# Optimization experiments

Hardware: AMD Instinct MI355X
Metric: run time of the kernel (lower is better)

## Reference

```python
import jax, jax.numpy as jnp
import numpy as np

B = 1
H_IMG, W_IMG = 64, 64
NF = H_IMG * W_IMG          # 4096 front/query tokens
NS = 1024                   # satellite tokens (32x32 grid)
SAT_IN, FRONT_IN = 768, 320
NH, HD = 8, 64
MD = NH * HD                # 512
GHID, GHD = 128, 16
GMD = NH * GHD              # 128
GEO_RATIO, ROPE_BASE = 0.5, 10000.0
LAMBDA_GEO, LAMBDA_GEOM = 1.0, 1.0
EPS = 1e-5


def _linear(x, w, b):
    return x @ w.T + b


def _layernorm(x, g, b):
    m = x.mean(-1, keepdims=True)
    v = jnp.var(x, axis=-1, keepdims=True)
    return (x - m) / jnp.sqrt(v + EPS) * g + b


def _georope(t, xy):
    """Continuous 2D (x,y) rotary embedding on the first GEO_RATIO fraction of head_dim.
    t: [B,NH,N,HD], xy: [B,N,2]."""
    rot = int(HD * GEO_RATIO)       # rotated dims (32)
    axis = rot // 2                 # dims per spatial axis (16)
    half = axis // 2                # frequency pairs per axis (8)
    inv_freq = ROPE_BASE ** (-jnp.arange(half, dtype=t.dtype) / half)

    def rot_axis(a, coord):
        th = coord[:, None, :, None] * inv_freq   # [B,1,N,half]
        c, s = jnp.cos(th), jnp.sin(th)
        a1, a2 = a[..., :half], a[..., half:]
        return jnp.concatenate([a1 * c - a2 * s, a1 * s + a2 * c], axis=-1)

    tx = rot_axis(t[..., :axis], xy[..., 0])
    ty = rot_axis(t[..., axis:rot], xy[..., 1])
    return jnp.concatenate([tx, ty, t[..., rot:]], axis=-1)


def _heads(x, hd):
    b, n, _ = x.shape
    return x.reshape(b, n, NH, hd).transpose(0, 2, 1, 3)


def setup_inputs() -> dict:
    key = jax.random.key(0)
    ks = iter(jax.random.split(key, 64))

    def w(*shape):
        return jax.random.normal(next(ks), shape, jnp.float32) / np.sqrt(shape[-1]).astype(np.float32)

    z = lambda n: jnp.zeros((n,), jnp.float32)
    o = lambda n: jnp.ones((n,), jnp.float32)
    return {
        "front_feat": jax.random.normal(next(ks), (B, FRONT_IN, H_IMG, W_IMG), jnp.float32),
        "front_bev_xy": jax.random.uniform(next(ks), (B, NF, 2), jnp.float32, -1.0, 1.0),
        "sat_tokens": jax.random.normal(next(ks), (B, NS, SAT_IN), jnp.float32),
        "sat_xy": jax.random.uniform(next(ks), (B, NS, 2), jnp.float32, -1.0, 1.0),
        "front_plucker": jax.random.normal(next(ks), (B, NF, 6), jnp.float32),
        "pos_w1": w(MD, 2), "pos_b1": z(MD), "pos_w2": w(MD, MD), "pos_b2": z(MD),
        "fa_w": w(MD, FRONT_IN), "fa_b": z(MD), "fa_ln_g": o(MD), "fa_ln_b": z(MD),
        "qn_g": o(MD), "qn_b": z(MD),
        "sa_w": w(MD, SAT_IN), "sa_b": z(MD), "sa_ln_g": o(MD), "sa_ln_b": z(MD),
        "wq": w(MD, MD), "bq": z(MD), "wk": w(MD, MD), "bk": z(MD), "wv": w(MD, MD), "bv": z(MD),
        "plk_w1": w(GHID, 6), "plk_b1": z(GHID), "plk_w2": w(GHID, GHID), "plk_b2": z(GHID),
        "sxy_w1": w(GHID, 2), "sxy_b1": z(GHID), "sxy_w2": w(GHID, GHID), "sxy_b2": z(GHID),
        "gqn_g": o(GHID), "gqn_b": z(GHID), "gkn_g": o(GHID), "gkn_b": z(GHID),
        "wqg": w(GMD, GHID), "bqg": z(GMD), "wkg": w(GMD, GHID), "bkg": z(GMD),
    }


def reference(front_feat, front_bev_xy, sat_tokens, sat_xy, front_plucker,
              pos_w1, pos_b1, pos_w2, pos_b2, fa_w, fa_b, fa_ln_g, fa_ln_b,
              qn_g, qn_b, sa_w, sa_b, sa_ln_g, sa_ln_b, wq, bq, wk, bk, wv, bv,
              plk_w1, plk_b1, plk_w2, plk_b2, sxy_w1, sxy_b1, sxy_w2, sxy_b2,
              gqn_g, gqn_b, gkn_g, gkn_b, wqg, bqg, wkg, bkg):
    b = front_feat.shape[0]
    ff = front_feat.reshape(b, FRONT_IN, NF).transpose(0, 2, 1)      # [B,NF,C]
    pos = _linear(jax.nn.silu(_linear(front_bev_xy, pos_w1, pos_b1)), pos_w2, pos_b2)
    feat = _layernorm(_linear(ff, fa_w, fa_b), fa_ln_g, fa_ln_b)
    q_embed = _layernorm(pos + feat, qn_g, qn_b)
    sat_feat = _layernorm(_linear(sat_tokens, sa_w, sa_b), sa_ln_g, sa_ln_b)
    q = _heads(_linear(q_embed, wq, bq), HD)                         # [B,H,NF,HD]
    k = _heads(_linear(sat_feat, wk, bk), HD)                        # [B,H,NS,HD]
    v = _heads(_linear(sat_feat, wv, bv), HD)
    qr = _georope(q, front_bev_xy)
    kr = _georope(k, sat_xy)
    logits = jnp.einsum('bhqd,bhkd->bhqk', qr, kr) / np.float32(np.sqrt(HD))
    # learned geometric Q/K stream (Plucker rays vs sat xy)
    plk = _layernorm(_linear(jax.nn.silu(_linear(front_plucker, plk_w1, plk_b1)), plk_w2, plk_b2), gqn_g, gqn_b)
    sgf = _layernorm(_linear(jax.nn.silu(_linear(sat_xy, sxy_w1, sxy_b1)), sxy_w2, sxy_b2), gkn_g, gkn_b)
    qg = _heads(_linear(plk, wqg, bqg), GHD)
    kg = _heads(_linear(sgf, wkg, bkg), GHD)
    logits = logits + LAMBDA_GEOM * (jnp.einsum('bhqd,bhkd->bhqk', qg, kg) / np.float32(np.sqrt(GHD)))
    # additive pairwise squared-distance bias, broadcast over heads
    dist2 = ((front_bev_xy[:, :, None, :] - sat_xy[:, None, :, :]) ** 2).sum(-1)   # [B,NF,NS]
    logits = logits - LAMBDA_GEO * dist2[:, None]
    attn = jax.nn.softmax(logits, axis=-1)
    read = jnp.einsum('bhqk,bhkd->bhqd', attn, v)
    return read.transpose(0, 2, 1, 3).reshape(b, NF, MD)
```

## Files before the change

kernel.cpp:

```cpp
#include <hip/hip_runtime.h>
#include <hip/hip_bf16.h>
#include <stdint.h>

#define NF 4096
#define NS 1024
#define MD 512
#define HD 64
#define DA 96
#define GHID 128

#define L2E 1.44269504f
#define S2L 1.6986436f

typedef unsigned short u16;
typedef __attribute__((ext_vector_type(8))) short bf8v;
typedef __attribute__((ext_vector_type(4))) float f4v;

__device__ __forceinline__ u16 f2bf(float f) {
  __hip_bfloat16 h = __float2bfloat16(f);
  return __builtin_bit_cast(u16, h);
}
__device__ __forceinline__ float bf2f(u16 u) {
  union { unsigned u; float f; } v; v.u = ((unsigned)u) << 16; return v.f;
}
__device__ __forceinline__ f4v mfma16(bf8v a, bf8v b, f4v c) {
  return __builtin_amdgcn_mfma_f32_16x16x32_bf16(a, b, c, 0, 0, 0);
}
__device__ __forceinline__ void gld16(const void* g, void* l) {
  __builtin_amdgcn_global_load_lds(
      (const __attribute__((address_space(1))) unsigned int*)g,
      (__attribute__((address_space(3))) unsigned int*)l, 16, 0, 0);
}

#define OFF_POSW2 0
#define OFF_FAW   262144
#define OFF_SAW   425984
#define OFF_WQ    819200
#define OFF_WKV   1081344
#define OFF_PLKW2 1605632
#define OFF_SXYW2 1622016
#define OFF_WQG   1638400
#define OFF_WKG   1654784
#define OFF_SATT  1671168
#define TOTW      2457600

__global__ __launch_bounds__(256) void k_l0(
    const float* __restrict__ s0, const float* __restrict__ s1,
    const float* __restrict__ s2, const float* __restrict__ s3,
    const float* __restrict__ s4, const float* __restrict__ s5,
    const float* __restrict__ s6, const float* __restrict__ s7,
    const float* __restrict__ s8, const float* __restrict__ s9,
    const float* __restrict__ s10, u16* __restrict__ pool,
    const float* __restrict__ bk, const float* __restrict__ bv,
    float* __restrict__ bkv,
    const float* __restrict__ ff, u16* __restrict__ ffT,
    const float* __restrict__ in0, const float* __restrict__ w0,
    const float* __restrict__ b0, u16* __restrict__ o0,
    const float* __restrict__ in1, const float* __restrict__ w1,
    const float* __restrict__ b1, u16* __restrict__ o1,
    const float* __restrict__ in2, const float* __restrict__ w2,
    const float* __restrict__ b2, u16* __restrict__ o2) {
  __shared__ u16 sT[32][72];
  int blk = blockIdx.x, t = threadIdx.x;
  if (blk < 2401) {
    int i4 = blk * 256 + t;
    if (i4 < TOTW / 4) {
      int idx = i4 * 4;
      const float* src; int off;
      if      (idx < OFF_FAW)   { src = s0;  off = OFF_POSW2; }
      else if (idx < OFF_SAW)   { src = s1;  off = OFF_FAW; }
      else if (idx < OFF_WQ)    { src = s2;  off = OFF_SAW; }
      else if (idx < OFF_WKV)   { src = s3;  off = OFF_WQ; }
      else if (idx < 1343488)   { src = s4;  off = OFF_WKV; }
      else if (idx < OFF_PLKW2) { src = s5;  off = 1343488; }
      else if (idx < OFF_SXYW2) { src = s6;  off = OFF_PLKW2; }
      else if (idx < OFF_WQG)   { src = s7;  off = OFF_SXYW2; }
      else if (idx < OFF_WKG)   { src = s8;  off = OFF_WQG; }
      else if (idx < OFF_SATT)  { src = s9;  off = OFF_WKG; }
      else                      { src = s10; off = OFF_SATT; }
      float4 v = *(const float4*)(src + (idx - off));
      ushort4 o;
      o.x = f2bf(v.x); o.y = f2bf(v.y); o.z = f2bf(v.z); o.w = f2bf(v.w);
      *(ushort4*)(pool + idx) = o;
    } else if (i4 < TOTW / 4 + 256) {
      int j = (i4 - TOTW / 4) * 4;
#pragma unroll
      for (int e = 0; e < 4; ++e) {
        int b = j + e;
        bkv[b] = (b < 512) ? bk[b] : bv[b - 512];
      }
    }
  } else if (blk < 3041) {
    int lb = blk - 2401;
    int n0 = (lb & 63) * 64, c0 = (lb >> 6) * 32;
    {
      int cr = t >> 3, nc = (t & 7) * 8;
      const float* src = ff + (size_t)(c0 + cr) * NF + n0 + nc;
      float4 v0 = *(const float4*)src, v1 = *(const float4*)(src + 4);
      bf8v p;
      p[0]=(short)f2bf(v0.x); p[1]=(short)f2bf(v0.y); p[2]=(short)f2bf(v0.z); p[3]=(short)f2bf(v0.w);
      p[4]=(short)f2bf(v1.x); p[5]=(short)f2bf(v1.y); p[6]=(short)f2bf(v1.z); p[7]=(short)f2bf(v1.w);
      *(bf8v*)&sT[cr][nc] = p;
    }
    __syncthreads();
    {
      int r = t >> 2, cc = (t & 3) * 8;
      bf8v p;
#pragma unroll
      for (int e = 0; e < 8; ++e) p[e] = (short)sT[cc + e][r];
      *(bf8v*)(ffT + (size_t)(n0 + r) * 320 + c0 + cc) = p;
    }
  } else {
    int lb = blk - 3041;
    const float *in, *w, *b; u16* o; int mlog, K, idx;
    if (lb < 8192)       { in = in0; w = w0; b = b0; o = o0; mlog = 9; K = 2; idx = lb * 256 + t; }
    else if (lb < 10240) { in = in1; w = w1; b = b1; o = o1; mlog = 7; K = 6; idx = (lb - 8192) * 256 + t; }
    else                 { in = in2; w = w2; b = b2; o = o2; mlog = 7; K = 2; idx = (lb - 10240) * 256 + t; }
    int M = 1 << mlog;
    int n = idx >> mlog, m = idx & (M - 1);
    float acc = b[m];
    for (int k = 0; k < K; ++k) acc += in[n * K + k] * w[m * K + k];
    o[idx] = f2bf(acc / (1.f + __expf(-acc)));
  }
}

__device__ __forceinline__ void gemm_body(const u16* __restrict__ A, const u16* __restrict__ W,
                                          const float* __restrict__ bias, u16* __restrict__ out,
                                          int m0, int n0, int N, int K) {
  constexpr int BM = 64, BN = 64;
  constexpr int MR = 2, NR = 2;
  __shared__ u16 sA[2][BM * 64];
  __shared__ u16 sB[2][BN * 64];
  const int tid = threadIdx.x, w = tid >> 6, lane = tid & 63;
  const int l16 = lane & 15, lh = lane >> 4;
  const int wr = w >> 1, wc = w & 1;

  f4v acc[MR][NR];
#pragma unroll
  for (int m = 0; m < MR; ++m)
#pragma unroll
    for (int j = 0; j < NR; ++j) acc[m][j] = (f4v){0.f, 0.f, 0.f, 0.f};

  auto stageA = [&](int buf, int k0) {
#pragma unroll
    for (int i = 0; i < 2; ++i) {
      int c = i * 256 + tid;
      int row = c >> 3, cp = c & 7;
      int sc_ = cp ^ (row & 7);
      gld16(A + (size_t)(m0 + row) * K + k0 + sc_ * 8, &sA[buf][c * 8]);
    }
  };
  auto stageB = [&](int buf, int k0) {
#pragma unroll
    for (int i = 0; i < 2; ++i) {
      int c = i * 256 + tid;
      int row = c >> 3, cp = c & 7;
      int sc_ = cp ^ (row & 7);
      gld16(W + (size_t)(n0 + row) * K + k0 + sc_ * 8, &sB[buf][c * 8]);
    }
  };

  stageA(0, 0); stageB(0, 0);
  __syncthreads();
  const int NK = K >> 6;
  for (int ks = 0; ks < NK; ++ks) {
    int nb = ks & 1;
    if (ks + 1 < NK) { stageA(nb ^ 1, (ks + 1) * 64); stageB(nb ^ 1, (ks + 1) * 64); }
#pragma unroll
    for (int kk = 0; kk < 2; ++kk) {
      bf8v af[MR], bfr[NR];
#pragma unroll
      for (int m = 0; m < MR; ++m) {
        int row = wr * 32 + m * 16 + l16;
        int cp = (kk * 4 + lh) ^ (row & 7);
        af[m] = *(const bf8v*)&sA[nb][row * 64 + cp * 8];
      }
#pragma unroll
      for (int j = 0; j < NR; ++j) {
        int row = wc * 32 + j * 16 + l16;
        int cp = (kk * 4 + lh) ^ (row & 7);
        bfr[j] = *(const bf8v*)&sB[nb][row * 64 + cp * 8];
      }
#pragma unroll
      for (int m = 0; m < MR; ++m)
#pragma unroll
        for (int j = 0; j < NR; ++j) acc[m][j] = mfma16(af[m], bfr[j], acc[m][j]);
    }
    __syncthreads();
  }
#pragma unroll
  for (int m = 0; m < MR; ++m) {
    int grow = m0 + wr * 32 + m * 16 + (lh << 2);
#pragma unroll
    for (int j = 0; j < NR; ++j) {
      int gcol = n0 + wc * 32 + j * 16 + l16;
      float bv = bias ? bias[gcol] : 0.f;
#pragma unroll
      for (int r = 0; r < 4; ++r)
        out[(size_t)(grow + r) * N + gcol] = f2bf(acc[m][j][r] + bv);
    }
  }
}

struct GP { const u16* A; const u16* W; const float* bias; u16* out; int K; int N; int M; };

__device__ __forceinline__ void gemm_dispatch(const GP& g, int blk) {
  int mt = g.M >> 6;
  int m0 = (blk % mt) * 64, n0 = (blk / mt) * 64;
  gemm_body(g.A, g.W, g.bias, g.out, m0, n0, g.N, g.K);
}

__global__ __launch_bounds__(256) void k_gemm_L1(GP a, GP b, GP c, GP d, GP e) {
  int blk = blockIdx.x;
  if (blk < 512)       gemm_dispatch(a, blk);
  else if (blk < 1024) gemm_dispatch(b, blk - 512);
  else if (blk < 1152) gemm_dispatch(c, blk - 1024);
  else if (blk < 1280) gemm_dispatch(d, blk - 1152);
  else                 gemm_dispatch(e, blk - 1280);
}
__global__ __launch_bounds__(256) void k_gemm_L2(GP a, GP b, GP c, GP d) {
  int blk = blockIdx.x;
  if (blk < 512)      gemm_dispatch(a, blk);
  else if (blk < 768) gemm_dispatch(b, blk - 512);
  else if (blk < 896) gemm_dispatch(c, blk - 768);
  else                gemm_dispatch(d, blk - 896);
}

__global__ __launch_bounds__(256) void k_ln_all(
    const u16* __restrict__ feat_pre, const u16* __restrict__ pos,
    const float* __restrict__ fg, const float* __restrict__ fb,
    const float* __restrict__ qg, const float* __restrict__ qb2,
    u16* __restrict__ q_embed,
    const u16* __restrict__ satf_pre, const float* __restrict__ sg,
    const float* __restrict__ sb, u16* __restrict__ satf,
    const u16* __restrict__ ginq, const u16* __restrict__ gink,
    const float* __restrict__ ggq, const float* __restrict__ gbq,
    const float* __restrict__ ggk, const float* __restrict__ gbk,
    u16* __restrict__ goutq, u16* __restrict__ goutk) {
  int blk = blockIdx.x;
  int w = threadIdx.x >> 6, lane = threadIdx.x & 63;
  if (blk < 1024) {
    int row = blk * 4 + w;
    bf8v v = *(const bf8v*)(feat_pre + (size_t)row * 512 + lane * 8);
    float x[8];
#pragma unroll
    for (int e = 0; e < 8; ++e) x[e] = bf2f((u16)v[e]);
    float s = 0.f, q = 0.f;
#pragma unroll
    for (int e = 0; e < 8; ++e) { s += x[e]; q += x[e] * x[e]; }
#pragma unroll
    for (int mm = 1; mm < 64; mm <<= 1) { s += __shfl_xor(s, mm); q += __shfl_xor(q, mm); }
    float mean = s / 512.f, var = q / 512.f - mean * mean;
    float rstd = rsqrtf(var + 1e-5f);
    bf8v vp = *(const bf8v*)(pos + (size_t)row * 512 + lane * 8);
#pragma unroll
    for (int e = 0; e < 8; ++e)
      x[e] = (x[e] - mean) * rstd * fg[lane * 8 + e] + fb[lane * 8 + e] + bf2f((u16)vp[e]);
    s = 0.f; q = 0.f;
#pragma unroll
    for (int e = 0; e < 8; ++e) { s += x[e]; q += x[e] * x[e]; }
#pragma unroll
    for (int mm = 1; mm < 64; mm <<= 1) { s += __shfl_xor(s, mm); q += __shfl_xor(q, mm); }
    mean = s / 512.f; var = q / 512.f - mean * mean;
    rstd = rsqrtf(var + 1e-5f);
    bf8v ov;
#pragma unroll
    for (int e = 0; e < 8; ++e)
      ov[e] = (short)f2bf((x[e] - mean) * rstd * qg[lane * 8 + e] + qb2[lane * 8 + e]);
    *(bf8v*)(q_embed + (size_t)row * 512 + lane * 8) = ov;
  } else if (blk < 1280) {
    int row = (blk - 1024) * 4 + w;
    bf8v v = *(const bf8v*)(satf_pre + (size_t)row * 512 + lane * 8);
    float x[8];
#pragma unroll
    for (int e = 0; e < 8; ++e) x[e] = bf2f((u16)v[e]);
    float s = 0.f, q = 0.f;
#pragma unroll
    for (int e = 0; e < 8; ++e) { s += x[e]; q += x[e] * x[e]; }
#pragma unroll
    for (int mm = 1; mm < 64; mm <<= 1) { s += __shfl_xor(s, mm); q += __shfl_xor(q, mm); }
    float mean = s / 512.f, var = q / 512.f - mean * mean;
    float rstd = rsqrtf(var + 1e-5f);
    bf8v ov;
#pragma unroll
    for (int e = 0; e < 8; ++e)
      ov[e] = (short)f2bf((x[e] - mean) * rstd * sg[lane * 8 + e] + sb[lane * 8 + e]);
    *(bf8v*)(satf + (size_t)row * 512 + lane * 8) = ov;
  } else {
    int row = (blk - 1280) * 4 + w;
    const u16* in; const float *g, *b; u16* out;
    if (row < 4096) { in = ginq; g = ggq; b = gbq; out = goutq; }
    else { row -= 4096; in = gink; g = ggk; b = gbk; out = goutk; }
    uint32_t v = *(const uint32_t*)(in + (size_t)row * 128 + lane * 2);
    float x0 = bf2f((u16)(v & 0xffff)), x1 = bf2f((u16)(v >> 16));
    float s = x0 + x1, q = x0 * x0 + x1 * x1;
#pragma unroll
    for (int mm = 1; mm < 64; mm <<= 1) { s += __shfl_xor(s, mm); q += __shfl_xor(q, mm); }
    float mean = s / 128.f, var = q / 128.f - mean * mean;
    float rstd = rsqrtf(var + 1e-5f);
    u16 o0 = f2bf((x0 - mean) * rstd * g[lane * 2] + b[lane * 2]);
    u16 o1 = f2bf((x1 - mean) * rstd * g[lane * 2 + 1] + b[lane * 2 + 1]);
    *(uint32_t*)(out + (size_t)row * 128 + lane * 2) = (uint32_t)o0 | ((uint32_t)o1 << 16);
  }
}

__global__ __launch_bounds__(256) void k_prep(
    const u16* __restrict__ qlin, const u16* __restrict__ qglin,
    const float* __restrict__ qxy, u16* __restrict__ Qaug_,
    const u16* __restrict__ klin, const u16* __restrict__ kglin,
    const float* __restrict__ kxy, u16* __restrict__ Kaug_,
    float* __restrict__ kk2_, u16* __restrict__ VT) {
  __shared__ u16 sT[64][72];
  int blk = blockIdx.x;
  if (blk < 10240) {
    int gid = blk * 4 + (threadIdx.x >> 6);
    int lane = threadIdx.x & 63;
    const u16 *lin, *glin; const float* xy; u16* aug;
    int lstride, n, h, isQ; float scm, scg;
    if (gid < NF * 8) {
      lin = qlin; glin = qglin; xy = qxy; aug = Qaug_;
      lstride = MD; n = gid >> 3; h = gid & 7; isQ = 1;
      scm = 0.125f * L2E; scg = 0.25f * L2E;
    } else {
      gid -= NF * 8;
      lin = klin; glin = kglin; xy = kxy; aug = Kaug_;
      lstride = 1024; n = gid >> 3; h = gid & 7; isQ = 0;
      scm = 1.f; scg = 1.f;
    }
    float val = bf2f(lin[(size_t)n * lstride + h * 64 + lane]);
    float part = __shfl_xor(val, 8);
    float x = xy[n * 2], y = xy[n * 2 + 1];
    float outv = val;
    if (lane < 32) {
      float coord = (lane < 16) ? x : y;
      int j = lane & 7;
      float th = coord * __expf(-(float)j * 1.1512925465f);
      float sn, cs;
      __sincosf(th, &sn, &cs);
      outv = ((lane & 8) == 0) ? (val * cs - part * sn) : (part * sn + val * cs);
    }
    u16* dst = aug + (size_t)(h * (isQ ? NF : NS) + n) * DA;
    dst[lane] = f2bf(outv * scm);
    if (lane < 16) {
      float gv = bf2f(glin[(size_t)n * GHID + h * 16 + lane]);
      dst[64 + lane] = f2bf(gv * scg);
    } else if (lane == 16) {
      dst[80] = f2bf(S2L * x);
    } else if (lane == 17) {
      dst[81] = f2bf(S2L * y);
    } else if (lane == 18) {
      dst[82] = 0;
      if (!isQ && h == 0) kk2_[n] = L2E * (x * x + y * y);
    } else if (lane < 32) {
      dst[64 + lane] = 0;
    }
  } else {
    int lb = blk - 10240;
    int n0 = (lb & 15) * 64, h = lb >> 4;
    int t = threadIdx.x;
    int r = t >> 2, c = (t & 3) * 16;
    const u16* src = klin + (size_t)(n0 + r) * 1024 + 512 + h * 64 + c;
    *(bf8v*)&sT[r][c]     = *(const bf8v*)src;
    *(bf8v*)&sT[r][c + 8] = *(const bf8v*)(src + 8);
    __syncthreads();
    int d = t >> 2, nc = (t & 3) * 16;
    bf8v p0, p1;
#pragma unroll
    for (int e = 0; e < 8; ++e) { p0[e] = (short)sT[nc + e][d]; p1[e] = (short)sT[nc + 8 + e][d]; }
    u16* dst = VT + (size_t)(h * 64 + d) * 1024 + n0 + nc;
    *(bf8v*)dst = p0;
    *(bf8v*)(dst + 8) = p1;
  }
}

__global__ __launch_bounds__(256, 4) void k_flash(const u16* __restrict__ Qa,
                                                  const u16* __restrict__ Ka,
                                                  const u16* __restrict__ VT,
                                                  const float* __restrict__ kk2,
                                                  float* __restrict__ Opart,
                                                  float2* __restrict__ ml) {
  const int h = blockIdx.y, qb = blockIdx.x, sp = blockIdx.z;
  const int tid = threadIdx.x, w = tid >> 6, lane = tid & 63;
  const int l16 = lane & 15, lh = lane >> 4;
  __shared__ u16 sK[64][104];
  __shared__ u16 sV[64][72];
  __shared__ u16 sP[4][16][72];
  __shared__ float sKK[512];

  ((float2*)sKK)[tid] = ((const float2*)(kk2 + sp * 512))[tid];

  const int qrow = qb * 64 + w * 16 + l16;
  bf8v qf[3];
#pragma unroll
  for (int c = 0; c < 3; ++c)
    qf[c] = *(const bf8v*)(Qa + (size_t)(h * NF + qrow) * DA + c * 32 + lh * 8);

  bf8v ONES;
#pragma unroll
  for (int i = 0; i < 8; ++i) ONES[i] = (short)0x3F80;

  const int crow = qb * 64 + w * 16 + (lh << 2);
  float m_run[4], l_run[4];
  f4v accO[4];
#pragma unroll
  for (int r = 0; r < 4; ++r) { m_run[r] = -1e30f; l_run[r] = 0.f; }
#pragma unroll
  for (int d = 0; d < 4; ++d) accO[d] = (f4v){0.f, 0.f, 0.f, 0.f};

  const int kt0 = sp * 8;
  bf8v kreg[3], vreg[2];
  auto sload = [&](int t8) {
    int kb = (kt0 + t8) * 64;
#pragma unroll
    for (int i = 0; i < 3; ++i) {
      int c = tid + i * 256; int r = c / 12, off = (c % 12) * 8;
      kreg[i] = *(const bf8v*)(Ka + ((size_t)(h * NS) + kb + r) * DA + off);
    }
#pragma unroll
    for (int i = 0; i < 2; ++i) {
      int c = tid + i * 256; int d = c >> 3, off = (c & 7) * 8;
      vreg[i] = *(const bf8v*)(VT + ((size_t)(h * HD) + d) * NS + kb + off);
    }
  };
  auto swrite = [&]() {
#pragma unroll
    for (int i = 0; i < 3; ++i) {
      int c = tid + i * 256; int r = c / 12, off = (c % 12) * 8;
      *(bf8v*)&sK[r][off] = kreg[i];
    }
#pragma unroll
    for (int i = 0; i < 2; ++i) {
      int c = tid + i * 256; int d = c >> 3, off = (c & 7) * 8;
      *(bf8v*)&sV[d][off] = vreg[i];
    }
  };

  sload(0); swrite();
  __syncthreads();
  for (int t8 = 0; t8 < 8; ++t8) {
    if (t8 < 7) sload(t8 + 1);
    float p[4][4];
    float rmax[4] = {-1e30f, -1e30f, -1e30f, -1e30f};
#pragma unroll
    for (int j = 0; j < 4; ++j) {
      f4v s4 = (f4v){0.f, 0.f, 0.f, 0.f};
#pragma unroll
      for (int c = 0; c < 3; ++c) {
        bf8v kf = *(const bf8v*)&sK[j * 16 + l16][c * 32 + lh * 8];
        s4 = mfma16(qf[c], kf, s4);
      }
      float ck = sKK[t8 * 64 + j * 16 + l16];
#pragma unroll
      for (int r = 0; r < 4; ++r) {
        float sv = s4[r] - ck;
        p[j][r] = sv;
        rmax[r] = fmaxf(rmax[r], sv);
      }
    }
#pragma unroll
    for (int r = 0; r < 4; ++r)
#pragma unroll
      for (int mm = 1; mm < 16; mm <<= 1)
        rmax[r] = fmaxf(rmax[r], __shfl_xor(rmax[r], mm));
    bool within = (rmax[0] <= m_run[0] + 8.f) && (rmax[1] <= m_run[1] + 8.f) &&
                  (rmax[2] <= m_run[2] + 8.f) && (rmax[3] <= m_run[3] + 8.f);
    if (!__all(within)) {
      float sc[4];
#pragma unroll
      for (int r = 0; r < 4; ++r) {
        float mnew = fmaxf(m_run[r], rmax[r]);
        sc[r] = exp2f(m_run[r] - mnew);
        m_run[r] = mnew;
      }
#pragma unroll
      for (int r = 0; r < 4; ++r) {
        l_run[r] *= sc[r];
#pragma unroll
        for (int d = 0; d < 4; ++d) accO[d][r] *= sc[r];
      }
    }
#pragma unroll
    for (int j = 0; j < 4; ++j)
#pragma unroll
      for (int r = 0; r < 4; ++r) {
        p[j][r] = exp2f(p[j][r] - m_run[r]);
        sP[w][(lh << 2) + r][j * 16 + l16] = f2bf(p[j][r]);
      }
    bf8v pf0 = *(const bf8v*)&sP[w][l16][lh * 8];
    bf8v pf1 = *(const bf8v*)&sP[w][l16][32 + lh * 8];
    f4v ls = (f4v){0.f, 0.f, 0.f, 0.f};
    ls = mfma16(pf0, ONES, ls);
    ls = mfma16(pf1, ONES, ls);
#pragma unroll
    for (int r = 0; r < 4; ++r) l_run[r] += ls[r];
#pragma unroll
    for (int c = 0; c < 2; ++c) {
      bf8v pf = (c == 0) ? pf0 : pf1;
#pragma unroll
      for (int d = 0; d < 4; ++d) {
        bf8v vf = *(const bf8v*)&sV[d * 16 + l16][c * 32 + lh * 8];
        accO[d] = mfma16(pf, vf, accO[d]);
      }
    }
    __syncthreads();
    if (t8 < 7) swrite();
    __syncthreads();
  }
  size_t obase = (size_t)(sp * 8 + h) * NF + crow;
#pragma unroll
  for (int d = 0; d < 4; ++d)
#pragma unroll
    for (int r = 0; r < 4; ++r)
      Opart[(obase + r) * 64 + d * 16 + l16] = accO[d][r];
  if (l16 == 0) {
#pragma unroll
    for (int r = 0; r < 4; ++r) ml[obase + r] = make_float2(m_run[r], l_run[r]);
  }
}

__global__ void k_combine(const float* __restrict__ Opart, const float2* __restrict__ ml,
                          float* __restrict__ out) {
  int i4 = blockIdx.x * 256 + threadIdx.x;
  int n = i4 >> 7;
  int c4 = i4 & 127, h = c4 >> 4, d4 = c4 & 15;
  float2 a = ml[(size_t)h * NF + n];
  float2 b = ml[(size_t)(8 + h) * NF + n];
  float m = fmaxf(a.x, b.x);
  float w1 = exp2f(a.x - m), w2 = exp2f(b.x - m);
  float rl = 1.f / (a.y * w1 + b.y * w2);
  float4 o1 = ((const float4*)(Opart + ((size_t)h * NF + n) * 64))[d4];
  float4 o2 = ((const float4*)(Opart + ((size_t)(8 + h) * NF + n) * 64))[d4];
  float4 r;
  r.x = (o1.x * w1 + o2.x * w2) * rl;
  r.y = (o1.y * w1 + o2.y * w2) * rl;
  r.z = (o1.z * w1 + o2.z * w2) * rl;
  r.w = (o1.w * w1 + o2.w * w2) * rl;
  ((float4*)out)[i4] = r;
}

extern "C" void kernel_launch(void* const* d_in, const int* in_sizes, int n_in,
                              void* d_out, int out_size, void* d_ws, size_t ws_size,
                              hipStream_t stream) {
  (void)in_sizes; (void)n_in; (void)out_size; (void)ws_size;
  const float* front_feat = (const float*)d_in[0];
  const float* bev_xy     = (const float*)d_in[1];
  const float* sat_tokens = (const float*)d_in[2];
  const float* sat_xy     = (const float*)d_in[3];
  const float* plucker    = (const float*)d_in[4];
  const float* pos_w1 = (const float*)d_in[5];
  const float* pos_b1 = (const float*)d_in[6];
  const float* pos_w2 = (const float*)d_in[7];
  const float* pos_b2 = (const float*)d_in[8];
  const float* fa_w   = (const float*)d_in[9];
  const float* fa_b   = (const float*)d_in[10];
  const float* fa_ln_g = (const float*)d_in[11];
  const float* fa_ln_b = (const float*)d_in[12];
  const float* qn_g   = (const float*)d_in[13];
  const float* qn_b   = (const float*)d_in[14];
  const float* sa_w   = (const float*)d_in[15];
  const float* sa_b   = (const float*)d_in[16];
  const float* sa_ln_g = (const float*)d_in[17];
  const float* sa_ln_b = (const float*)d_in[18];
  const float* wq = (const float*)d_in[19];
  const float* bq = (const float*)d_in[20];
  const float* wk = (const float*)d_in[21];
  const float* bk = (const float*)d_in[22];
  const float* wv = (const float*)d_in[23];
  const float* bv = (const float*)d_in[24];
  const float* plk_w1 = (const float*)d_in[25];
  const float* plk_b1 = (const float*)d_in[26];
  const float* plk_w2 = (const float*)d_in[27];
  const float* plk_b2 = (const float*)d_in[28];
  const float* sxy_w1 = (const float*)d_in[29];
  const float* sxy_b1 = (const float*)d_in[30];
  const float* sxy_w2 = (const float*)d_in[31];
  const float* sxy_b2 = (const float*)d_in[32];
  const float* gqn_g = (const float*)d_in[33];
  const float* gqn_b = (const float*)d_in[34];
  const float* gkn_g = (const float*)d_in[35];
  const float* gkn_b = (const float*)d_in[36];
  const float* wqg = (const float*)d_in[37];
  const float* bqg = (const float*)d_in[38];
  const float* wkg = (const float*)d_in[39];
  const float* bkg = (const float*)d_in[40];

  char* ws = (char*)d_ws;
  size_t off = 0;
  auto alloc = [&](size_t bytes) {
    size_t r = off;
    off += (bytes + 255) & ~(size_t)255;
    return r;
  };
  u16*   wpool   = (u16*)(ws + alloc((size_t)TOTW * 2));
  float* bkv     = (float*)(ws + alloc(1024 * 4));
  u16*   ffT     = (u16*)(ws + alloc((size_t)NF * 320 * 2));
  u16*   pos_h   = (u16*)(ws + alloc((size_t)NF * MD * 2));
  u16*   plk_h   = (u16*)(ws + alloc((size_t)NF * GHID * 2));
  u16*   sxy_h   = (u16*)(ws + alloc((size_t)NS * GHID * 2));
  u16*   pos     = (u16*)(ws + alloc((size_t)NF * MD * 2));
  u16*   feat_pre= (u16*)(ws + alloc((size_t)NF * MD * 2));
  u16*   satf_pre= (u16*)(ws + alloc((size_t)NS * MD * 2));
  u16*   satf    = (u16*)(ws + alloc((size_t)NS * MD * 2));
  u16*   q_embed = (u16*)(ws + alloc((size_t)NF * MD * 2));
  u16*   plk2    = (u16*)(ws + alloc((size_t)NF * GHID * 2));
  u16*   sxy2    = (u16*)(ws + alloc((size_t)NS * GHID * 2));
  u16*   q_lin   = (u16*)(ws + alloc((size_t)NF * MD * 2));
  u16*   kv_lin  = (u16*)(ws + alloc((size_t)NS * 1024 * 2));
  u16*   Qaug    = (u16*)(ws + alloc((size_t)8 * NF * DA * 2));
  u16*   Kaug    = (u16*)(ws + alloc((size_t)8 * NS * DA * 2));
  u16*   VT      = (u16*)(ws + alloc((size_t)8 * HD * NS * 2));
  float* kk2     = (float*)(ws + alloc((size_t)NS * 4));
  float* Opart   = (float*)(ws + alloc((size_t)2 * 8 * NF * 64 * 4));
  float2* mlb    = (float2*)(ws + alloc((size_t)2 * 8 * NF * 8));
  u16* plk_ln = plk_h;
  u16* sgf    = sxy_h;
  u16* qg_lin = plk2;
  u16* kg_lin = sxy2;

  dim3 b256(256);
  k_l0<<<dim3(13793), b256, 0, stream>>>(
      pos_w2, fa_w, sa_w, wq, wk, wv, plk_w2, sxy_w2, wqg, wkg, sat_tokens,
      wpool, bk, bv, bkv, front_feat, ffT,
      bev_xy, pos_w1, pos_b1, pos_h,
      plucker, plk_w1, plk_b1, plk_h,
      sat_xy, sxy_w1, sxy_b1, sxy_h);

  GP gpos {pos_h, wpool + OFF_POSW2, pos_b2, pos, 512, 512, 4096};
  GP gfeat{ffT, wpool + OFF_FAW, fa_b, feat_pre, 320, 512, 4096};
  GP gsat {wpool + OFF_SATT, wpool + OFF_SAW, sa_b, satf_pre, 768, 512, 1024};
  GP ggq1 {plk_h, wpool + OFF_PLKW2, plk_b2, plk2, 128, 128, 4096};
  GP ggk1 {sxy_h, wpool + OFF_SXYW2, sxy_b2, sxy2, 128, 128, 1024};
  k_gemm_L1<<<dim3(1312), b256, 0, stream>>>(gpos, gfeat, gsat, ggq1, ggk1);

  k_ln_all<<<dim3(2560), b256, 0, stream>>>(
      feat_pre, pos, fa_ln_g, fa_ln_b, qn_g, qn_b, q_embed,
      satf_pre, sa_ln_g, sa_ln_b, satf,
      plk2, sxy2, gqn_g, gqn_b, gkn_g, gkn_b, plk_ln, sgf);

  GP gq  {q_embed, wpool + OFF_WQ, bq, q_lin, 512, 512, 4096};
  GP gkv {satf, wpool + OFF_WKV, bkv, kv_lin, 512, 1024, 1024};
  GP ggq2{plk_ln, wpool + OFF_WQG, bqg, qg_lin, 128, 128, 4096};
  GP ggk2{sgf, wpool + OFF_WKG, bkg, kg_lin, 128, 128, 1024};
  k_gemm_L2<<<dim3(928), b256, 0, stream>>>(gq, gkv, ggq2, ggk2);

  k_prep<<<dim3(10368), b256, 0, stream>>>(
      q_lin, qg_lin, bev_xy, Qaug, kv_lin, kg_lin, sat_xy, Kaug, kk2, VT);

  k_flash<<<dim3(NF / 64, 8, 2), b256, 0, stream>>>(Qaug, Kaug, VT, kk2, Opart, mlb);
  k_combine<<<dim3(NF * MD / 4 / 256), b256, 0, stream>>>(Opart, mlb, (float*)d_out);
}
```

Baseline: 92.63 us.

## Enlarge GEMM tiles to 128x128 with 32-wide K steps and new swizzle

The batched GEMM kernels now compute 128x128 output tiles per block, with each wave holding a 4x4 grid of MFMA accumulators instead of 2x2, and step K by 32 using a new LDS XOR swizzle. This raises reuse of the staged A and B fragments and cuts redundant global loads. The grids are rebuilt accordingly and put the long-K sat and kv GEMMs first in dispatch order. In exchange the block count falls to a few hundred, which may underfill the MI355X's CUs, and the larger accumulator set raises register pressure.

```diff
diff --git a/kernel.cpp b/kernel.cpp
--- a/kernel.cpp
+++ b/kernel.cpp
@@ -127,73 +127,63 @@
 __device__ __forceinline__ void gemm_body(const u16* __restrict__ A, const u16* __restrict__ W,
                                           const float* __restrict__ bias, u16* __restrict__ out,
                                           int m0, int n0, int N, int K) {
-  constexpr int BM = 64, BN = 64;
-  constexpr int MR = 2, NR = 2;
-  __shared__ u16 sA[2][BM * 64];
-  __shared__ u16 sB[2][BN * 64];
+  __shared__ u16 sA[2][128 * 32];
+  __shared__ u16 sB[2][128 * 32];
   const int tid = threadIdx.x, w = tid >> 6, lane = tid & 63;
   const int l16 = lane & 15, lh = lane >> 4;
   const int wr = w >> 1, wc = w & 1;
 
-  f4v acc[MR][NR];
-#pragma unroll
-  for (int m = 0; m < MR; ++m)
-#pragma unroll
-    for (int j = 0; j < NR; ++j) acc[m][j] = (f4v){0.f, 0.f, 0.f, 0.f};
-
-  auto stageA = [&](int buf, int k0) {
+  f4v acc[4][4];
+#pragma unroll
+  for (int m = 0; m < 4; ++m)
+#pragma unroll
+    for (int j = 0; j < 4; ++j) acc[m][j] = (f4v){0.f, 0.f, 0.f, 0.f};
+
+  auto stage = [&](const u16* __restrict__ src, u16* dst, int r0, int k0, int K_) {
 #pragma unroll
     for (int i = 0; i < 2; ++i) {
       int c = i * 256 + tid;
-      int row = c >> 3, cp = c & 7;
-      int sc_ = cp ^ (row & 7);
-      gld16(A + (size_t)(m0 + row) * K + k0 + sc_ * 8, &sA[buf][c * 8]);
+      int row = c >> 2, s = c & 3;
+      int g = s ^ ((row ^ (row >> 2)) & 3);
+      gld16(src + (size_t)(r0 + row) * K_ + k0 + g * 8, dst + c * 8);
     }
   };
-  auto stageB = [&](int buf, int k0) {
-#pragma unroll
-    for (int i = 0; i < 2; ++i) {
-      int c = i * 256 + tid;
-      int row = c >> 3, cp = c & 7;
-      int sc_ = cp ^ (row & 7);
-      gld16(W + (size_t)(n0 + row) * K + k0 + sc_ * 8, &sB[buf][c * 8]);
-    }
-  };
-
-  stageA(0, 0); stageB(0, 0);
+
+  stage(A, sA[0], m0, 0, K);
+  stage(W, sB[0], n0, 0, K);
   __syncthreads();
-  const int NK = K >> 6;
+  const int NK = K >> 5;
   for (int ks = 0; ks < NK; ++ks) {
     int nb = ks & 1;
-    if (ks + 1 < NK) { stageA(nb ^ 1, (ks + 1) * 64); stageB(nb ^ 1, (ks + 1) * 64); }
-#pragma unroll
-    for (int kk = 0; kk < 2; ++kk) {
-      bf8v af[MR], bfr[NR];
-#pragma unroll
-      for (int m = 0; m < MR; ++m) {
-        int row = wr * 32 + m * 16 + l16;
-        int cp = (kk * 4 + lh) ^ (row & 7);
-        af[m] = *(const bf8v*)&sA[nb][row * 64 + cp * 8];
-      }
-#pragma unroll
-      for (int j = 0; j < NR; ++j) {
-        int row = wc * 32 + j * 16 + l16;
-        int cp = (kk * 4 + lh) ^ (row & 7);
-        bfr[j] = *(const bf8v*)&sB[nb][row * 64 + cp * 8];
-      }
-#pragma unroll
-      for (int m = 0; m < MR; ++m)
-#pragma unroll
-        for (int j = 0; j < NR; ++j) acc[m][j] = mfma16(af[m], bfr[j], acc[m][j]);
-    }
+    if (ks + 1 < NK) {
+      stage(A, sA[nb ^ 1], m0, (ks + 1) * 32, K);
+      stage(W, sB[nb ^ 1], n0, (ks + 1) * 32, K);
+    }
+    bf8v af[4], bfr[4];
+#pragma unroll
+    for (int m = 0; m < 4; ++m) {
+      int row = wr * 64 + m * 16 + l16;
+      int s = lh ^ ((row ^ (row >> 2)) & 3);
+      af[m] = *(const bf8v*)&sA[nb][row * 32 + s * 8];
+    }
+#pragma unroll
+    for (int j = 0; j < 4; ++j) {
+      int row = wc * 64 + j * 16 + l16;
+      int s = lh ^ ((row ^ (row >> 2)) & 3);
+      bfr[j] = *(const bf8v*)&sB[nb][row * 32 + s * 8];
+    }
+#pragma unroll
+    for (int m = 0; m < 4; ++m)
+#pragma unroll
+      for (int j = 0; j < 4; ++j) acc[m][j] = mfma16(af[m], bfr[j], acc[m][j]);
     __syncthreads();
   }
 #pragma unroll
-  for (int m = 0; m < MR; ++m) {
-    int grow = m0 + wr * 32 + m * 16 + (lh << 2);
-#pragma unroll
-    for (int j = 0; j < NR; ++j) {
-      int gcol = n0 + wc * 32 + j * 16 + l16;
+  for (int m = 0; m < 4; ++m) {
+    int grow = m0 + wr * 64 + m * 16 + (lh << 2);
+#pragma unroll
+    for (int j = 0; j < 4; ++j) {
+      int gcol = n0 + wc * 64 + j * 16 + l16;
       float bv = bias ? bias[gcol] : 0.f;
 #pragma unroll
       for (int r = 0; r < 4; ++r)
@@ -205,25 +195,25 @@
 struct GP { const u16* A; const u16* W; const float* bias; u16* out; int K; int N; int M; };
 
 __device__ __forceinline__ void gemm_dispatch(const GP& g, int blk) {
-  int mt = g.M >> 6;
-  int m0 = (blk % mt) * 64, n0 = (blk / mt) * 64;
+  int mt = g.M >> 7;
+  int m0 = (blk % mt) * 128, n0 = (blk / mt) * 128;
   gemm_body(g.A, g.W, g.bias, g.out, m0, n0, g.N, g.K);
 }
 
-__global__ __launch_bounds__(256) void k_gemm_L1(GP a, GP b, GP c, GP d, GP e) {
+__global__ __launch_bounds__(256) void k_gemm_L1(GP sat, GP pos, GP feat, GP gq, GP gk) {
   int blk = blockIdx.x;
-  if (blk < 512)       gemm_dispatch(a, blk);
-  else if (blk < 1024) gemm_dispatch(b, blk - 512);
-  else if (blk < 1152) gemm_dispatch(c, blk - 1024);
-  else if (blk < 1280) gemm_dispatch(d, blk - 1152);
-  else                 gemm_dispatch(e, blk - 1280);
-}
-__global__ __launch_bounds__(256) void k_gemm_L2(GP a, GP b, GP c, GP d) {
+  if (blk < 32)        gemm_dispatch(sat, blk);
+  else if (blk < 160)  gemm_dispatch(pos, blk - 32);
+  else if (blk < 288)  gemm_dispatch(feat, blk - 160);
+  else if (blk < 320)  gemm_dispatch(gq, blk - 288);
+  else                 gemm_dispatch(gk, blk - 320);
+}
+__global__ __launch_bounds__(256) void k_gemm_L2(GP kv, GP q, GP gq, GP gk) {
   int blk = blockIdx.x;
-  if (blk < 512)      gemm_dispatch(a, blk);
-  else if (blk < 768) gemm_dispatch(b, blk - 512);
-  else if (blk < 896) gemm_dispatch(c, blk - 768);
-  else                gemm_dispatch(d, blk - 896);
+  if (blk < 64)        gemm_dispatch(kv, blk);
+  else if (blk < 192)  gemm_dispatch(q, blk - 64);
+  else if (blk < 224)  gemm_dispatch(gq, blk - 192);
+  else                 gemm_dispatch(gk, blk - 224);
 }
 
 __global__ __launch_bounds__(256) void k_ln_all(
@@ -625,23 +615,23 @@
       plucker, plk_w1, plk_b1, plk_h,
       sat_xy, sxy_w1, sxy_b1, sxy_h);
 
+  GP gsat {wpool + OFF_SATT, wpool + OFF_SAW, sa_b, satf_pre, 768, 512, 1024};
   GP gpos {pos_h, wpool + OFF_POSW2, pos_b2, pos, 512, 512, 4096};
   GP gfeat{ffT, wpool + OFF_FAW, fa_b, feat_pre, 320, 512, 4096};
-  GP gsat {wpool + OFF_SATT, wpool + OFF_SAW, sa_b, satf_pre, 768, 512, 1024};
   GP ggq1 {plk_h, wpool + OFF_PLKW2, plk_b2, plk2, 128, 128, 4096};
   GP ggk1 {sxy_h, wpool + OFF_SXYW2, sxy_b2, sxy2, 128, 128, 1024};
-  k_gemm_L1<<<dim3(1312), b256, 0, stream>>>(gpos, gfeat, gsat, ggq1, ggk1);
+  k_gemm_L1<<<dim3(328), b256, 0, stream>>>(gsat, gpos, gfeat, ggq1, ggk1);
 
   k_ln_all<<<dim3(2560), b256, 0, stream>>>(
       feat_pre, pos, fa_ln_g, fa_ln_b, qn_g, qn_b, q_embed,
       satf_pre, sa_ln_g, sa_ln_b, satf,
       plk2, sxy2, gqn_g, gqn_b, gkn_g, gkn_b, plk_ln, sgf);
 
+  GP gkv {satf, wpool + OFF_WKV, bkv, kv_lin, 512, 1024, 1024};
   GP gq  {q_embed, wpool + OFF_WQ, bq, q_lin, 512, 512, 4096};
-  GP gkv {satf, wpool + OFF_WKV, bkv, kv_lin, 512, 1024, 1024};
   GP ggq2{plk_ln, wpool + OFF_WQG, bqg, qg_lin, 128, 128, 4096};
   GP ggk2{sgf, wpool + OFF_WKG, bkg, kg_lin, 128, 128, 1024};
-  k_gemm_L2<<<dim3(928), b256, 0, stream>>>(gq, gkv, ggq2, ggk2);
+  k_gemm_L2<<<dim3(232), b256, 0, stream>>>(gkv, gq, ggq2, ggk2);
 
   k_prep<<<dim3(10368), b256, 0, stream>>>(
       q_lin, qg_lin, bev_xy, Qaug, kv_lin, kg_lin, sat_xy, Kaug, kk2, VT);
```

New measurement: 103.9 us. 12.2% more time.
